# Optimization experiments

Measured on AMD Instinct MI355X. Metric: run time of the kernel, lower is better.

## Reference

```python
import jax, jax.numpy as jnp
import numpy as np

NUM_SUB = (128, 32)
NUM_NEI = (24, 24)
LN_EPS = 1e-5


def bilinear(fmap, pts):
    # fmap: [C,H,W]; pts: [P,2] as (y,x) normalized to [0,1]; align_corners=True
    C, H, W = fmap.shape
    gy = pts[:, 0] * (H - 1)
    gx = pts[:, 1] * (W - 1)
    y0 = jnp.floor(gy)
    x0 = jnp.floor(gx)
    wy = gy - y0
    wx = gx - x0
    y0i = jnp.clip(y0.astype(jnp.int32), 0, H - 1)
    y1i = jnp.clip(y0i + 1, 0, H - 1)
    x0i = jnp.clip(x0.astype(jnp.int32), 0, W - 1)
    x1i = jnp.clip(x0i + 1, 0, W - 1)
    v00 = fmap[:, y0i, x0i]
    v01 = fmap[:, y0i, x1i]
    v10 = fmap[:, y1i, x0i]
    v11 = fmap[:, y1i, x1i]
    out = (v00 * (1 - wy) * (1 - wx) + v01 * (1 - wy) * wx
           + v10 * wy * (1 - wx) + v11 * wy * wx)
    return out.T  # [P,C]


def fps(xyz, npoint):
    # farthest point sampling, deterministic start at index 0. xyz: [B,N,2]
    B, N, _ = xyz.shape
    bidx = jnp.arange(B)

    def step(carry, _):
        dist, far = carry
        c = xyz[bidx, far][:, None, :]            # [B,1,2]
        d = jnp.sum((xyz - c) ** 2, -1)           # [B,N]
        dist = jnp.minimum(dist, d)
        return (dist, jnp.argmax(dist, -1)), far

    init = (jnp.full((B, N), 1e10, xyz.dtype), jnp.zeros((B,), jnp.int32))
    _, idx = jax.lax.scan(step, init, None, length=npoint)
    return idx.T  # [B,npoint]


def sqdist(a, b):
    # a: [B,S,2], b: [B,N,2] -> [B,S,N]
    return (jnp.sum(a ** 2, -1)[..., None] + jnp.sum(b ** 2, -1)[:, None, :]
            - 2.0 * jnp.einsum('bsc,bnc->bsn', a, b))


def layernorm(x, g, b):
    m = jnp.mean(x, -1, keepdims=True)
    v = jnp.mean((x - m) ** 2, -1, keepdims=True)
    return (x - m) / jnp.sqrt(v + LN_EPS) * g + b


def setup_inputs() -> dict:
    key = jax.random.key(0)
    ks = jax.random.split(key, 8)
    B, N, C, H, W = 32, 512, 1024, 24, 24
    Dp = C + 2
    out_dim = 4096
    return {
        'feature_map': jax.random.normal(ks[0], (B, C, H, W), jnp.float32),
        'points': jax.random.uniform(ks[1], (B, N, 2), jnp.float32),
        'W_diff': jax.random.normal(ks[2], (2, Dp, Dp), jnp.float32) * 0.02,
        'b_diff': jnp.zeros((2, Dp), jnp.float32),
        'W_agg': jax.random.normal(ks[3], (2, C, 2 * Dp), jnp.float32) * 0.02,
        'b_agg': jnp.zeros((2, C), jnp.float32),
        'ln_g': jnp.ones((2, C), jnp.float32),
        'ln_b': jnp.zeros((2, C), jnp.float32),
        'W_flat': jax.random.normal(ks[4], (C, C * NUM_SUB[-1]), jnp.float32) * 0.02,
        'b_flat': jnp.zeros((C,), jnp.float32),
        'W_dim': jax.random.normal(ks[5], (out_dim, C), jnp.float32) * 0.02,
        'b_dim': jnp.zeros((out_dim,), jnp.float32),
    }


def reference(feature_map, points, W_diff, b_diff, W_agg, b_agg,
              ln_g, ln_b, W_flat, b_flat, W_dim, b_dim):
    B = points.shape[0]
    all_pts = points                              # [B,N,2]
    all_fea = jax.vmap(bilinear)(feature_map, points)  # [B,N,C]
    bidx = jnp.arange(B)[:, None, None]
    for i, (S, K) in enumerate(zip(NUM_SUB, NUM_NEI)):
        fi = fps(all_pts, S)                                   # [B,S]
        new_pts = jnp.take_along_axis(all_pts, fi[..., None], 1)   # [B,S,2]
        new_fea = jnp.take_along_axis(all_fea, fi[..., None], 1)   # [B,S,C]
        d2 = sqdist(new_pts, all_pts)                          # [B,S,N]
        _, idx = jax.lax.top_k(-d2, K)                         # [B,S,K]
        grp_pts = all_pts[bidx, idx]                           # [B,S,K,2]
        grp_fea = all_fea[bidx, idx]                           # [B,S,K,C]
        local = jnp.concatenate([grp_fea, grp_pts], -1)        # [B,S,K,C+2]
        anchor = jnp.concatenate([new_fea, new_pts], -1)[:, :, None, :]
        diff = jnp.einsum('bskd,od->bsko', local - anchor, W_diff[i]) + b_diff[i]
        gath = jnp.concatenate([diff, jnp.broadcast_to(anchor, diff.shape)], -1)
        # Conv1d(kernel=1) + ReLU + LayerNorm over channels
        h = jax.nn.relu(jnp.einsum('bskd,od->bsko', gath, W_agg[i]) + b_agg[i])
        h = layernorm(h, ln_g[i], ln_b[i])
        all_pts, all_fea = new_pts, jnp.mean(h, 2)             # mean pool over K
    x = all_fea.reshape(B, -1)
    x = x @ W_flat.T + b_flat
    return x @ W_dim.T + b_dim
```

## Files before the change

kernel.cpp:

```cpp
#include <hip/hip_runtime.h>


typedef float f32x4 __attribute__((ext_vector_type(4)));
typedef short bf16x8 __attribute__((ext_vector_type(8)));
typedef unsigned short u16;
typedef u16 u16x4 __attribute__((ext_vector_type(4)));
typedef unsigned int u32;
typedef u32 u32x4 __attribute__((ext_vector_type(4)));
typedef unsigned long long u64;

typedef const void __attribute__((address_space(1)))* gvp;
typedef void __attribute__((address_space(3)))* svp;

__device__ __forceinline__ u16 f2bf(float f) {
  union { float f; u32 u; } x; x.f = f;
  u32 r = x.u + 0x7fffu + ((x.u >> 16) & 1u);
  return (u16)(r >> 16);
}

#define KP 1056
#define NP0 1152

__device__ __forceinline__ float rl_f(float v, int lane) {
  return __int_as_float(__builtin_amdgcn_readlane(__float_as_int(v), lane));
}

template <int CTRL>
__device__ __forceinline__ float dpp_fmax(float v) {
  float o = __int_as_float(__builtin_amdgcn_update_dpp(
      (int)0xff800000 , __float_as_int(v), CTRL, 0xf, 0xf, false));
  return fmaxf(v, o);
}

template <int CTRL>
__device__ __forceinline__ float dpp_fmin(float v) {
  float o = __int_as_float(__builtin_amdgcn_update_dpp(
      0x7f800000 , __float_as_int(v), CTRL, 0xf, 0xf, false));
  return fminf(v, o);
}

template <int CTRL>
__device__ __forceinline__ float dpp_add(float v) {
  float o = __int_as_float(__builtin_amdgcn_update_dpp(
      0, __float_as_int(v), CTRL, 0xf, 0xf, false));
  return v + o;
}

__device__ __forceinline__ float wave_fmax63(float v) {
  v = dpp_fmax<0x111>(v);
  v = dpp_fmax<0x112>(v);
  v = dpp_fmax<0x114>(v);
  v = dpp_fmax<0x118>(v);
  v = dpp_fmax<0x142>(v);
  v = dpp_fmax<0x143>(v);
  return rl_f(v, 63);
}

__device__ __forceinline__ float wave_fmin63(float v) {
  v = dpp_fmin<0x111>(v);
  v = dpp_fmin<0x112>(v);
  v = dpp_fmin<0x114>(v);
  v = dpp_fmin<0x118>(v);
  v = dpp_fmin<0x142>(v);
  v = dpp_fmin<0x143>(v);
  return rl_f(v, 63);
}

__device__ __forceinline__ float wave_sum63(float v) {
  v = dpp_add<0x111>(v);
  v = dpp_add<0x112>(v);
  v = dpp_add<0x114>(v);
  v = dpp_add<0x118>(v);
  v = dpp_add<0x142>(v);
  v = dpp_add<0x143>(v);
  return v;
}

template <int PPL, int HS>
__device__ void fps_core(const float* __restrict__ pts, int* __restrict__ fi,
                         int Np, int S, int b, int lane, int s0, int s1,
                         float* __restrict__ dsave, int* __restrict__ fsave) {
  #pragma clang fp contract(off)
  float px[PPL], py[PPL], dist[PPL];
  #pragma unroll
  for (int j = 0; j < PPL; ++j) {
    int n = j * 64 + lane;
    px[j] = pts[((size_t)b * Np + n) * 2];
    py[j] = pts[((size_t)b * Np + n) * 2 + 1];
  }
  int far; float cx, cy;
  if (s0 == 0) {
    #pragma unroll
    for (int j = 0; j < PPL; ++j) dist[j] = 1e10f;
    far = 0;
    cx = rl_f(px[0], 0);
    cy = rl_f(py[0], 0);
  } else {
    #pragma unroll
    for (int j = 0; j < PPL; ++j) dist[j] = dsave[(size_t)b * Np + j * 64 + lane];
    far = fsave[b];
    cx = pts[((size_t)b * Np + far) * 2];
    cy = pts[((size_t)b * Np + far) * 2 + 1];
  }
  int hist[HS];
  #pragma unroll
  for (int h = 0; h < HS; ++h) hist[h] = 0;
  for (int s = s0; s < s1; ++s) {
    #pragma unroll
    for (int h = 0; h < HS; ++h)
      if ((s >> 6) == h && (s & 63) == lane) hist[h] = far;
    float tv[PPL]; int ti[PPL]; float tx[PPL], ty[PPL];
    #pragma unroll
    for (int j = 0; j < PPL; ++j) {
      float dx = px[j] - cx, dy = py[j] - cy;
      float d = dx * dx + dy * dy;
      float nd = fminf(dist[j], d);
      dist[j] = nd;
      tv[j] = nd; ti[j] = j * 64 + lane; tx[j] = px[j]; ty[j] = py[j];
    }
    #pragma unroll
    for (int w = PPL; w > 1; w >>= 1)
      #pragma unroll
      for (int j = 0; j < (w >> 1); ++j)
        if (tv[j + (w >> 1)] > tv[j]) {
          tv[j] = tv[j + (w >> 1)]; ti[j] = ti[j + (w >> 1)];
          tx[j] = tx[j + (w >> 1)]; ty[j] = ty[j + (w >> 1)];
        }
    float smax = wave_fmax63(tv[0]);
    u64 mask = __ballot(tv[0] == smax);
    int L = __builtin_ctzll(mask);
    int fidx = __builtin_amdgcn_readlane(ti[0], L);
    float fx = rl_f(tx[0], L), fy = rl_f(ty[0], L);
    u64 rest = mask & (mask - 1);
    if (__builtin_expect(rest != 0, 0)) {
      while (rest) {
        int L2 = __builtin_ctzll(rest);
        int c = __builtin_amdgcn_readlane(ti[0], L2);
        if (c < fidx) {
          fidx = c; fx = rl_f(tx[0], L2); fy = rl_f(ty[0], L2);
        }
        rest &= rest - 1;
      }
    }
    far = fidx; cx = fx; cy = fy;
  }
  if (s1 < S) {
    #pragma unroll
    for (int j = 0; j < PPL; ++j) dsave[(size_t)b * Np + j * 64 + lane] = dist[j];
    if (lane == 0) fsave[b] = far;
  }
  #pragma unroll
  for (int h = 0; h < HS; ++h) {
    int s = h * 64 + lane;
    if (s >= s0 && s < s1) fi[b * S + s] = hist[h];
  }
}

template <int PPL>
__device__ void knn_core(const float* __restrict__ qpts,
                         const float* __restrict__ rpts,
                         int* __restrict__ idxK, int Np, int S, int q, int lane) {
  #pragma clang fp contract(off)
  int b = q / S;
  float ax = qpts[(size_t)q * 2], ay = qpts[(size_t)q * 2 + 1];
  float a2 = ax * ax + ay * ay;
  float d2[PPL];
  #pragma unroll
  for (int j = 0; j < PPL; ++j) {
    int n = j * 64 + lane;
    float bx = rpts[((size_t)b * Np + n) * 2];
    float by = rpts[((size_t)b * Np + n) * 2 + 1];
    float b2 = bx * bx + by * by;
    float dot = ax * bx + ay * by;
    float t = a2 + b2;
    float m2 = 2.f * dot;
    d2[j] = t - m2;
  }
  int kreg = 0;
  for (int k = 0; k < 24; ++k) {
    float tv[PPL]; int ti[PPL];
    #pragma unroll
    for (int j = 0; j < PPL; ++j) { tv[j] = d2[j]; ti[j] = j * 64 + lane; }
    #pragma unroll
    for (int w = PPL; w > 1; w >>= 1)
      #pragma unroll
      for (int j = 0; j < (w >> 1); ++j)
        if (tv[j + (w >> 1)] < tv[j]) {
          tv[j] = tv[j + (w >> 1)]; ti[j] = ti[j + (w >> 1)];
        }
    float smin = wave_fmin63(tv[0]);
    u64 mask = __ballot(tv[0] == smin);
    int L = __builtin_ctzll(mask);
    int bs = __builtin_amdgcn_readlane(ti[0], L);
    u64 rest = mask & (mask - 1);
    if (__builtin_expect(rest != 0, 0)) {
      while (rest) {
        int L2 = __builtin_ctzll(rest);
        int c = __builtin_amdgcn_readlane(ti[0], L2);
        if (c < bs) bs = c;
        rest &= rest - 1;
      }
    }
    if (lane == k) kreg = bs;
    #pragma unroll
    for (int j = 0; j < PPL; ++j)
      if (j * 64 + lane == bs) d2[j] = 3.4e38f;
  }
  if (lane < 24) idxK[(size_t)q * 24 + lane] = kreg;
}

__global__ __launch_bounds__(256, 2) void bilinear_fused_kernel(const float* __restrict__ fmap,
                                                                const float* __restrict__ pts,
                                                                u16* __restrict__ X,
                                                                int* __restrict__ fi0,
                                                                float* __restrict__ fdist,
                                                                int* __restrict__ ffar) {
  if (blockIdx.y == 0) {
    if (blockIdx.x < 8)
      fps_core<8, 2>(pts, fi0, 512, 128, blockIdx.x * 4 + (threadIdx.x >> 6),
                     threadIdx.x & 63, 0, 48, fdist, ffar);
    return;
  }
  __shared__ float fmS[32][580];
  const int ct = blockIdx.x, b = blockIdx.y - 1;
  const int t = threadIdx.x;
  const float* src = fmap + ((size_t)b * 1024 + ct * 32) * 576;
  const int tr = t >> 3, ti = t & 7;
  #pragma unroll
  for (int j = 0; j < 18; ++j) {
    int c4 = j * 8 + ti;
    *(f32x4*)&fmS[tr][c4 * 4] = *(const f32x4*)(src + (size_t)tr * 576 + c4 * 4);
  }
  __syncthreads();
  #pragma unroll
  for (int pass = 0; pass < 2; ++pass) {
    const int n = pass * 256 + t;
    const int pidx = b * 512 + n;
    float p0 = pts[(size_t)pidx * 2], p1 = pts[(size_t)pidx * 2 + 1];
    float gy = p0 * 23.f, gx = p1 * 23.f;
    float y0f = floorf(gy), x0f = floorf(gx);
    float wy = gy - y0f, wx = gx - x0f;
    int y0 = (int)y0f; y0 = y0 < 0 ? 0 : (y0 > 23 ? 23 : y0);
    int x0 = (int)x0f; x0 = x0 < 0 ? 0 : (x0 > 23 ? 23 : x0);
    int y1 = y0 + 1 > 23 ? 23 : y0 + 1;
    int x1 = x0 + 1 > 23 ? 23 : x0 + 1;
    float w00 = (1.f - wy) * (1.f - wx), w01 = (1.f - wy) * wx;
    float w10 = wy * (1.f - wx), w11 = wy * wx;
    const int i00 = y0 * 24 + x0, i01 = y0 * 24 + x1;
    const int i10 = y1 * 24 + x0, i11 = y1 * 24 + x1;
    size_t ro = (size_t)pidx * KP + ct * 32;
    #pragma unroll
    for (int cq = 0; cq < 8; ++cq) {
      u16x4 o4;
      #pragma unroll
      for (int cc = 0; cc < 4; ++cc) {
        int c = cq * 4 + cc;
        float v = w00 * fmS[c][i00] + w01 * fmS[c][i01] +
                  w10 * fmS[c][i10] + w11 * fmS[c][i11];
        o4[cc] = f2bf(v);
      }
      *(u16x4*)(X + ro + cq * 4) = o4;
    }
    if (ct == 31) {
      size_t rb = (size_t)pidx * KP;
      X[rb + 1024] = f2bf(p0);
      X[rb + 1025] = f2bf(p1);
      #pragma unroll
      for (int z = 0; z < 15; ++z) ((u32*)(X + rb + 1026))[z] = 0;
    }
  }
}

__global__ __launch_bounds__(128) void gather_fi_kernel(const u16* __restrict__ Xsrc,
                                                        const float* __restrict__ pts,
                                                        const int* __restrict__ fi,
                                                        u16* __restrict__ Xg,
                                                        float* __restrict__ npts,
                                                        int Np, int S) {
  int q = blockIdx.x;
  int b = q / S;
  int t = threadIdx.x;
  int r = fi[q];
  const u32x4* src = (const u32x4*)(Xsrc + ((size_t)b * Np + r) * KP);
  u32x4* dst = (u32x4*)(Xg + (size_t)q * KP);
  dst[t] = src[t];
  int t2 = t + 128;
  if (t2 < 132) dst[t2] = src[t2];
  if (t == 0) {
    npts[(size_t)q * 2] = pts[((size_t)b * Np + r) * 2];
    npts[(size_t)q * 2 + 1] = pts[((size_t)b * Np + r) * 2 + 1];
  }
}

__global__ __launch_bounds__(256) void wd_transpose_kernel(const float* __restrict__ Wd,
                                                           u16* __restrict__ WdT) {
  __shared__ float tbuf[32][33];
  int tx = threadIdx.x & 31, ty = threadIdx.x >> 5;
  int ot = blockIdx.x * 32, dt = blockIdx.y * 32;
  #pragma unroll
  for (int j = 0; j < 4; ++j) {
    int o = ot + ty + 8 * j, d = dt + tx;
    tbuf[ty + 8 * j][tx] = (o < 1026 && d < 1026) ? Wd[(size_t)o * 1026 + d] : 0.f;
  }
  __syncthreads();
  #pragma unroll
  for (int j = 0; j < 4; ++j) {
    int d = dt + ty + 8 * j, o = ot + tx;
    if (o < KP) WdT[(size_t)d * KP + o] = f2bf(tbuf[tx][ty + 8 * j]);
  }
}

__global__ __launch_bounds__(256) void wagg_convert_kernel(const float* __restrict__ Wagg,
                                                           u16* __restrict__ Wa1,
                                                           u16* __restrict__ Wa2) {
  int c = blockIdx.x, t = threadIdx.x;
  const float* row = Wagg + (size_t)c * 2052;
  for (int d = t; d < KP; d += 256) {
    Wa1[(size_t)c * KP + d] = (d < 1026) ? f2bf(row[d]) : (u16)0;
    Wa2[(size_t)c * KP + d] = (d < 1026) ? f2bf(row[1026 + d]) : (u16)0;
  }
}

__global__ __launch_bounds__(256) void czero_kernel(const float* __restrict__ bdiff,
                                                    const float* __restrict__ Wagg,
                                                    const float* __restrict__ bagg,
                                                    float* __restrict__ czero) {
  int lane = threadIdx.x & 63, wv = threadIdx.x >> 6;
  int c = blockIdx.x * 4 + wv;
  float acc = 0.f;
  for (int o = lane; o < 1026; o += 64) acc += bdiff[o] * Wagg[(size_t)c * 2052 + o];
  #pragma unroll
  for (int off = 32; off; off >>= 1) acc += __shfl_xor(acc, off);
  if (lane == 0) czero[c] = acc + bagg[c];
}

template <int BF16OUT, int FPS_PPL, int FPS_HS, int SWZ, int KNN_PPL>
__global__ __launch_bounds__(256) void gemm_bt_kernel(const u16* __restrict__ A,
                                                      const u16* __restrict__ Bt,
                                                      void* __restrict__ Cout,
                                                      int M, int N, int K, int ldc, int nvalid,
                                                      const float* __restrict__ fpts,
                                                      int* __restrict__ ffi,
                                                      int fNp, int fS, int fs0, int fs1,
                                                      float* __restrict__ fdist,
                                                      int* __restrict__ ffar,
                                                      const float* __restrict__ kq,
                                                      const float* __restrict__ kr,
                                                      int* __restrict__ kidx,
                                                      int kNp, int kS, int kYoff) {
  const int tid = threadIdx.x;
  const int lane = tid & 63;
  const int wv = tid >> 6;
  const int FR = (FPS_PPL > 0) ? 1 : 0;
  if (FPS_PPL > 0 && blockIdx.y == 0) {
    if (blockIdx.x < 8)
      fps_core<FPS_PPL ? FPS_PPL : 1, FPS_HS>(fpts, ffi, fNp, fS,
                                              blockIdx.x * 4 + wv, lane, fs0, fs1,
                                              fdist, ffar);
    return;
  }
  if (KNN_PPL > 0 && (int)blockIdx.y >= kYoff) {
    int kb = ((int)blockIdx.y - kYoff) * gridDim.x + blockIdx.x;
    knn_core<KNN_PPL ? KNN_PPL : 1>(kq, kr, kidx, kNp, kS, kb * 4 + wv, lane);
    return;
  }
  __shared__ __align__(16) u16 As[128 * 32];
  __shared__ __align__(16) u16 Bs[128 * 32];
  int mt, nt;
  if (SWZ) {
    const int g = ((int)blockIdx.y - FR) * gridDim.x + blockIdx.x;
    const int MT = (KNN_PPL > 0 ? kYoff : (int)gridDim.y) - FR;
    const int cpx = MT >> 3;
    const int xcd = g & 7;
    const int r = g >> 3;
    mt = xcd * cpx + (r >> 3);
    nt = r & 7;
  } else {
    mt = (int)blockIdx.y - FR;
    nt = blockIdx.x;
  }
  const int m0 = mt * 128;
  const int n0 = nt * 128;
  const int wm = (wv >> 1) * 64;
  const int wn = (wv & 1) * 64;

  f32x4 acc[4][4];
  #pragma unroll
  for (int i = 0; i < 4; ++i)
    #pragma unroll
    for (int j = 0; j < 4; ++j)
      #pragma unroll
      for (int c = 0; c < 4; ++c) acc[i][j][c] = 0.f;

  const int ch0 = wv * 2;
  const int rin = lane >> 2;
  const int slot = lane & 3;
  const int cin = (slot ^ (rin & 3) ^ ((rin >> 2) & 3)) * 8;

  for (int k0 = 0; k0 < K; k0 += 32) {
    #pragma unroll
    for (int i = 0; i < 2; ++i) {
      const int ch = ch0 + i;
      const int row = ch * 16 + rin;
      const u16* ga = A + (size_t)(m0 + row) * K + (k0 + cin);
      const u16* gb = Bt + (size_t)(n0 + row) * K + (k0 + cin);
      __builtin_amdgcn_global_load_lds((gvp)ga, (svp)(As + ch * 512), 16, 0, 0);
      __builtin_amdgcn_global_load_lds((gvp)gb, (svp)(Bs + ch * 512), 16, 0, 0);
    }
    __syncthreads();
    const int rf = lane & 15;
    const int quad = lane >> 4;
    const int qs = (quad ^ (rf & 3) ^ ((rf >> 2) & 3)) * 8;
    bf16x8 af[4], bfv[4];
    #pragma unroll
    for (int mi = 0; mi < 4; ++mi)
      af[mi] = *(const bf16x8*)(As + (wm + mi * 16 + rf) * 32 + qs);
    #pragma unroll
    for (int ni = 0; ni < 4; ++ni)
      bfv[ni] = *(const bf16x8*)(Bs + (wn + ni * 16 + rf) * 32 + qs);
    #pragma unroll
    for (int mi = 0; mi < 4; ++mi)
      #pragma unroll
      for (int ni = 0; ni < 4; ++ni)
        acc[mi][ni] = __builtin_amdgcn_mfma_f32_16x16x32_bf16(af[mi], bfv[ni], acc[mi][ni], 0, 0, 0);
    __syncthreads();
  }

  const int rq = (lane >> 4) * 4;
  const int cf = lane & 15;
  #pragma unroll
  for (int mi = 0; mi < 4; ++mi) {
    #pragma unroll
    for (int ni = 0; ni < 4; ++ni) {
      const int col = n0 + wn + ni * 16 + cf;
      #pragma unroll
      for (int r = 0; r < 4; ++r) {
        const int row = m0 + wm + mi * 16 + rq + r;
        const float v = acc[mi][ni][r];
        if (BF16OUT) {
          if (col < nvalid) ((u16*)Cout)[(size_t)row * ldc + col] = f2bf(v);
        } else {
          ((float*)Cout)[(size_t)row * ldc + col] = v;
        }
      }
    }
  }
}

template <int MODE, int FPS_PPL, int FPS_HS>
__global__ __launch_bounds__(256) void h_epilogue_kernel(const float* __restrict__ Z1,
                                                         const float* __restrict__ Z2g,
                                                         const float* __restrict__ czero,
                                                         const int* __restrict__ idxK,
                                                         const int* __restrict__ fi,
                                                         const float* __restrict__ g,
                                                         const float* __restrict__ bb,
                                                         const float* __restrict__ npts,
                                                         void* __restrict__ outp,
                                                         int Np, int S, int cpx,
                                                         const float* __restrict__ fpts,
                                                         int* __restrict__ ffi,
                                                         int fNp, int fS) {
  const int t = threadIdx.x;
  const int lane = t & 63, wv = t >> 6;
  if (FPS_PPL > 0 && blockIdx.x < 8) {
    fps_core<FPS_PPL ? FPS_PPL : 1, FPS_HS>(fpts, ffi, fNp, fS,
                                            blockIdx.x * 4 + wv, lane, 0, fS,
                                            nullptr, nullptr);
    return;
  }
  const int bid = blockIdx.x - (FPS_PPL > 0 ? 8 : 0);
  const int sw = (bid & 7) * cpx + (bid >> 3);
  const int q = sw * 4 + wv;
  const int b = q / S;
  const int fiv = fi[q];
  const float* z2 = Z2g + (size_t)q * 1024;
  const float* zf = Z1 + ((size_t)b * Np + fiv) * 1024;
  const int ch = lane * 4;

  f32x4 base[4], gv[4], bv[4], acc[4];
  #pragma unroll
  for (int j = 0; j < 4; ++j) {
    f32x4 a = *(const f32x4*)(z2 + j * 256 + ch);
    f32x4 c = *(const f32x4*)(czero + j * 256 + ch);
    f32x4 f = *(const f32x4*)(zf + j * 256 + ch);
    #pragma unroll
    for (int c2 = 0; c2 < 4; ++c2) base[j][c2] = a[c2] + c[c2] - f[c2];
    gv[j] = *(const f32x4*)(g + j * 256 + ch);
    bv[j] = *(const f32x4*)(bb + j * 256 + ch);
    #pragma unroll
    for (int c2 = 0; c2 < 4; ++c2) acc[j][c2] = 0.f;
  }
  int nk = 0;
  if (lane < 24) nk = idxK[(size_t)q * 24 + lane];

  for (int k = 0; k < 24; ++k) {
    const int n = __builtin_amdgcn_readlane(nk, k);
    const float* zr = Z1 + ((size_t)b * Np + n) * 1024;
    f32x4 v[4];
    float s1 = 0.f, s2 = 0.f;
    #pragma unroll
    for (int j = 0; j < 4; ++j) {
      f32x4 r = *(const f32x4*)(zr + j * 256 + ch);
      #pragma unroll
      for (int c2 = 0; c2 < 4; ++c2) {
        float x = fmaxf(r[c2] + base[j][c2], 0.f);
        v[j][c2] = x;
        s1 += x;
        s2 += x * x;
      }
    }
    s1 = wave_sum63(s1);
    s2 = wave_sum63(s2);
    const float S1 = rl_f(s1, 63);
    const float S2 = rl_f(s2, 63);
    const float m = S1 * (1.f / 1024.f);
    const float var = S2 * (1.f / 1024.f) - m * m;
    const float rs = rsqrtf(var + 1e-5f);
    #pragma unroll
    for (int j = 0; j < 4; ++j)
      #pragma unroll
      for (int c2 = 0; c2 < 4; ++c2)
        acc[j][c2] += (v[j][c2] - m) * rs * gv[j][c2] + bv[j][c2];
  }

  u16x4 o4[4];
  #pragma unroll
  for (int j = 0; j < 4; ++j)
    #pragma unroll
    for (int c2 = 0; c2 < 4; ++c2) o4[j][c2] = f2bf(acc[j][c2] * (1.f / 24.f));

  if (MODE == 0) {
    u16* X = (u16*)outp;
    size_t ro = (size_t)q * KP;
    #pragma unroll
    for (int j = 0; j < 4; ++j) *(u16x4*)(X + ro + j * 256 + ch) = o4[j];
    if (lane == 0) {
      X[ro + 1024] = f2bf(npts[(size_t)q * 2]);
      X[ro + 1025] = f2bf(npts[(size_t)q * 2 + 1]);
    }
    if (lane < 15) ((u32*)(X + ro + 1026))[lane] = 0;
  } else {
    u16* X = (u16*)outp + (size_t)q * 1024;
    #pragma unroll
    for (int j = 0; j < 4; ++j) *(u16x4*)(X + j * 256 + ch) = o4[j];
  }
}

template <int KSBITS, int NST>
__global__ __launch_bounds__(256, 4) void mlp_mfma_kernel(const float* __restrict__ W,
                                                          const u16* __restrict__ Fb,
                                                          float* __restrict__ P, int K) {
  __shared__ __align__(16) float Asf[128 * 32];
  __shared__ __align__(16) u16 Fsb[32 * 40];
  const int tid = threadIdx.x, lane = tid & 63, wv = tid >> 6;
  const int ot = blockIdx.x >> KSBITS;
  const int ks = blockIdx.x & ((1 << KSBITS) - 1);
  const int m0 = ot * 128;
  const int k0b = ks * (NST * 32);
  const int arow = lane >> 3;
  const int agrp = lane & 7;
  const int rf = lane & 15, quad = lane >> 4;

  f32x4 acc[2][2];
  #pragma unroll
  for (int i = 0; i < 2; ++i)
    #pragma unroll
    for (int j = 0; j < 2; ++j)
      #pragma unroll
      for (int c = 0; c < 4; ++c) acc[i][j][c] = 0.f;

  for (int st = 0; st < NST; ++st) {
    const int k0 = k0b + st * 32;
    #pragma unroll
    for (int i = 0; i < 4; ++i) {
      const int row = wv * 32 + i * 8 + arow;
      const int g = agrp ^ (row & 7);
      const float* ga = W + (size_t)(m0 + row) * K + k0 + g * 4;
      __builtin_amdgcn_global_load_lds((gvp)ga, (svp)(Asf + (wv * 32 + i * 8) * 32), 16, 0, 0);
    }
    if (tid < 128) {
      const int fr = tid >> 2, fc = (tid & 3) * 8;
      u32x4 tmp = *(const u32x4*)(Fb + (size_t)fr * K + k0 + fc);
      *(u32x4*)(Fsb + fr * 40 + fc) = tmp;
    }
    __syncthreads();
    bf16x8 bfr[2];
    #pragma unroll
    for (int ni = 0; ni < 2; ++ni)
      bfr[ni] = *(const bf16x8*)(Fsb + (ni * 16 + rf) * 40 + quad * 8);
    #pragma unroll
    for (int mi = 0; mi < 2; ++mi) {
      const float* ap = Asf + (size_t)(wv * 32 + mi * 16 + rf) * 32;
      f32x4 a0 = *(const f32x4*)(ap + (((quad * 2) ^ (rf & 7)) * 4));
      f32x4 a1 = *(const f32x4*)(ap + (((quad * 2 + 1) ^ (rf & 7)) * 4));
      union { bf16x8 v; u16 h[8]; } af;
      #pragma unroll
      for (int c = 0; c < 4; ++c) { af.h[c] = f2bf(a0[c]); af.h[4 + c] = f2bf(a1[c]); }
      #pragma unroll
      for (int ni = 0; ni < 2; ++ni)
        acc[mi][ni] = __builtin_amdgcn_mfma_f32_16x16x32_bf16(af.v, bfr[ni], acc[mi][ni], 0, 0, 0);
    }
    __syncthreads();
  }

  float* Pb = P + (size_t)blockIdx.x * 4096;
  const int rq = (lane >> 4) * 4, cf = lane & 15;
  #pragma unroll
  for (int mi = 0; mi < 2; ++mi)
    #pragma unroll
    for (int ni = 0; ni < 2; ++ni)
      #pragma unroll
      for (int r = 0; r < 4; ++r)
        Pb[(wv * 32 + mi * 16 + rq + r) * 32 + ni * 16 + cf] = acc[mi][ni][r];
}

__global__ __launch_bounds__(256) void reduce_flat_kernel(const float* __restrict__ P,
                                                          const float* __restrict__ bias,
                                                          u16* __restrict__ x1bf) {
  int idx = blockIdx.x * 256 + threadIdx.x;
  int o = idx >> 5, b = idx & 31;
  float s = bias[o];
  const float* p = P + ((size_t)(o >> 7) * 64) * 4096 + (o & 127) * 32 + b;
  #pragma unroll 8
  for (int ks = 0; ks < 64; ++ks) s += p[(size_t)ks * 4096];
  x1bf[(size_t)b * 1024 + o] = f2bf(s);
}

__global__ __launch_bounds__(256) void reduce_dim_kernel(const float* __restrict__ P,
                                                         const float* __restrict__ bias,
                                                         float* __restrict__ out) {
  int idx = blockIdx.x * 256 + threadIdx.x;
  int o = idx >> 5, b = idx & 31;
  float s = bias[o];
  const float* p = P + ((size_t)(o >> 7) * 8) * 4096 + (o & 127) * 32 + b;
  #pragma unroll
  for (int ks = 0; ks < 8; ++ks) s += p[(size_t)ks * 4096];
  out[(size_t)b * 4096 + o] = s;
}

extern "C" void kernel_launch(void* const* d_in, const int* in_sizes, int n_in,
                              void* d_out, int out_size, void* d_ws, size_t ws_size,
                              hipStream_t stream) {
  const float* fmap  = (const float*)d_in[0];
  const float* pts   = (const float*)d_in[1];
  const float* Wdiff = (const float*)d_in[2];
  const float* bdiff = (const float*)d_in[3];
  const float* Wagg  = (const float*)d_in[4];
  const float* bagg  = (const float*)d_in[5];
  const float* lng   = (const float*)d_in[6];
  const float* lnb   = (const float*)d_in[7];
  const float* Wflat = (const float*)d_in[8];
  const float* bflat = (const float*)d_in[9];
  const float* Wdim  = (const float*)d_in[10];
  const float* bdim  = (const float*)d_in[11];
  float* out = (float*)d_out;

  char* w = (char*)d_ws;
  size_t off = 0;
  auto alloc = [&](size_t n) { char* p = w + off; off += (n + 255) & ~(size_t)255; return p; };

  float* Z1    = (float*)alloc(16384ull * 1024 * 4);
  float* Z2g   = (float*)alloc(4096ull * 1024 * 4);
  u16* Xbf0  = (u16*)alloc(16384ull * KP * 2);
  u16* X1bf  = (u16*)alloc(4096ull * KP * 2);
  u16* Xg    = (u16*)alloc(4096ull * KP * 2);
  u16* WdT   = (u16*)alloc((size_t)NP0 * KP * 2);
  u16* Wa1   = (u16*)alloc(1024ull * KP * 2);
  u16* Wa2   = (u16*)alloc(1024ull * KP * 2);
  u16* Wcomb = (u16*)alloc(1024ull * KP * 2);
  float* czero = (float*)alloc(1024 * 4);
  int* fi0   = (int*)alloc(32 * 128 * 4);
  int* fi1   = (int*)alloc(32 * 32 * 4);
  int* idx0  = (int*)alloc(32 * 128 * 24 * 4);
  int* idx1  = (int*)alloc(32 * 32 * 24 * 4);
  float* npts0 = (float*)alloc(32 * 128 * 2 * 4);
  float* npts1 = (float*)alloc(32 * 32 * 2 * 4);
  u16* fea2bf = (u16*)alloc(32ull * 32768 * 2);
  u16* x1bf   = (u16*)alloc(32ull * 1024 * 2);
  float* Pf   = (float*)alloc(512ull * 4096 * 4);
  float* Pd   = (float*)alloc(256ull * 4096 * 4);
  float* fdist = (float*)alloc(32ull * 512 * 4);
  int* ffar    = (int*)alloc(32 * 4);

  bilinear_fused_kernel<<<dim3(32, 33), 256, 0, stream>>>(fmap, pts, Xbf0, fi0, fdist, ffar);

  wd_transpose_kernel<<<dim3(33, 36), 256, 0, stream>>>(Wdiff, WdT);
  wagg_convert_kernel<<<1024, 256, 0, stream>>>(Wagg, Wa1, Wa2);
  czero_kernel<<<256, 256, 0, stream>>>(bdiff, Wagg, bagg, czero);
  gemm_bt_kernel<1, 0, 1, 0, 0><<<dim3(9, 8), 256, 0, stream>>>(
      Wa1, WdT, Wcomb, 1024, NP0, KP, KP, KP,
      nullptr, nullptr, 0, 0, 0, 0, nullptr, nullptr,
      nullptr, nullptr, nullptr, 0, 0, 0);
  gemm_bt_kernel<0, 8, 2, 1, 0><<<dim3(8, 129), 256, 0, stream>>>(
      Xbf0, Wcomb, Z1, 16384, 1024, KP, 1024, 1024,
      pts, fi0, 512, 128, 48, 128, fdist, ffar,
      nullptr, nullptr, nullptr, 0, 0, 0);
  gather_fi_kernel<<<4096, 128, 0, stream>>>(Xbf0, pts, fi0, Xg, npts0, 512, 128);
  gemm_bt_kernel<0, 0, 1, 1, 8><<<dim3(8, 160), 256, 0, stream>>>(
      Xg, Wa2, Z2g, 4096, 1024, KP, 1024, 1024,
      nullptr, nullptr, 0, 0, 0, 0, nullptr, nullptr,
      npts0, pts, idx0, 512, 128, 32);
  h_epilogue_kernel<0, 2, 1><<<1032, 256, 0, stream>>>(
      Z1, Z2g, czero, idx0, fi0, lng, lnb, npts0, X1bf, 512, 128, 128,
      npts0, fi1, 128, 32);

  wd_transpose_kernel<<<dim3(33, 36), 256, 0, stream>>>(Wdiff + 1026 * 1026, WdT);
  wagg_convert_kernel<<<1024, 256, 0, stream>>>(Wagg + 1024 * 2052, Wa1, Wa2);
  czero_kernel<<<256, 256, 0, stream>>>(bdiff + 1026, Wagg + 1024 * 2052, bagg + 1024, czero);
  gemm_bt_kernel<1, 0, 1, 0, 0><<<dim3(9, 8), 256, 0, stream>>>(
      Wa1, WdT, Wcomb, 1024, NP0, KP, KP, KP,
      nullptr, nullptr, 0, 0, 0, 0, nullptr, nullptr,
      nullptr, nullptr, nullptr, 0, 0, 0);
  gemm_bt_kernel<0, 0, 1, 1, 0><<<dim3(8, 32), 256, 0, stream>>>(
      X1bf, Wcomb, Z1, 4096, 1024, KP, 1024, 1024,
      nullptr, nullptr, 0, 0, 0, 0, nullptr, nullptr,
      nullptr, nullptr, nullptr, 0, 0, 0);
  gather_fi_kernel<<<1024, 128, 0, stream>>>(X1bf, npts0, fi1, Xg, npts1, 128, 32);
  gemm_bt_kernel<0, 0, 1, 1, 2><<<dim3(8, 40), 256, 0, stream>>>(
      Xg, Wa2, Z2g, 1024, 1024, KP, 1024, 1024,
      nullptr, nullptr, 0, 0, 0, 0, nullptr, nullptr,
      npts1, npts0, idx1, 128, 32, 8);
  h_epilogue_kernel<1, 0, 1><<<256, 256, 0, stream>>>(
      Z1, Z2g, czero, idx1, fi1, lng + 1024, lnb + 1024, npts1, fea2bf, 128, 32, 32,
      nullptr, nullptr, 0, 0);

  mlp_mfma_kernel<6, 16><<<512, 256, 0, stream>>>(Wflat, fea2bf, Pf, 32768);
  reduce_flat_kernel<<<128, 256, 0, stream>>>(Pf, bflat, x1bf);
  mlp_mfma_kernel<3, 4><<<256, 256, 0, stream>>>(Wdim, x1bf, Pd, 1024);
  reduce_dim_kernel<<<512, 256, 0, stream>>>(Pd, bdim, out);
}
```

Baseline: 623.9 us.

## Batch both stages' weight prep, fold row gather into GEMM, split FPS across kernels

Weight preprocessing for both stages (transpose, bf16 conversion, czero bias fold, Wcomb GEMM) is now done in fewer, batched launches. Stage-two weight prep no longer sits on the critical path between the stages. The separate gather_fi kernels are removed: the gather GEMMs index rows of the source activations through the FPS indices, and FPS writes the sampled point coordinates directly. The first-stage FPS is split into three segments (0-32, 32-56, 56-128) hidden behind the bilinear, Wcomb and first GEMM kernels. This trades fewer launches and less copy traffic for more scattered A-row loads and a larger weight workspace.

After: 551.4 us. 1.13x faster.

```diff
diff --git a/kernel.cpp b/kernel.cpp
--- a/kernel.cpp
+++ b/kernel.cpp
@@ -78,6 +78,7 @@
 
 template <int PPL, int HS>
 __device__ void fps_core(const float* __restrict__ pts, int* __restrict__ fi,
+                         float* __restrict__ npts,
                          int Np, int S, int b, int lane, int s0, int s1,
                          float* __restrict__ dsave, int* __restrict__ fsave) {
   #pragma clang fp contract(off)
@@ -152,7 +153,12 @@
   #pragma unroll
   for (int h = 0; h < HS; ++h) {
     int s = h * 64 + lane;
-    if (s >= s0 && s < s1) fi[b * S + s] = hist[h];
+    if (s >= s0 && s < s1) {
+      int hv = hist[h];
+      fi[b * S + s] = hv;
+      npts[(size_t)(b * S + s) * 2]     = pts[((size_t)b * Np + hv) * 2];
+      npts[(size_t)(b * S + s) * 2 + 1] = pts[((size_t)b * Np + hv) * 2 + 1];
+    }
   }
 }
 
@@ -209,16 +215,108 @@
   if (lane < 24) idxK[(size_t)q * 24 + lane] = kreg;
 }
 
+template <int BF16OUT, int IND>
+__device__ __forceinline__ void gemm_tile_body(const u16* __restrict__ A,
+                                               const u16* __restrict__ Bt,
+                                               void* __restrict__ Cout,
+                                               int K, int ldc, int nvalid,
+                                               int m0, int n0,
+                                               const int* __restrict__ find,
+                                               int iNp, int iS,
+                                               u16* __restrict__ As,
+                                               u16* __restrict__ Bs) {
+  const int tid = threadIdx.x;
+  const int lane = tid & 63;
+  const int wv = tid >> 6;
+  const int wm = (wv >> 1) * 64;
+  const int wn = (wv & 1) * 64;
+
+  f32x4 acc[4][4];
+  #pragma unroll
+  for (int i = 0; i < 4; ++i)
+    #pragma unroll
+    for (int j = 0; j < 4; ++j)
+      #pragma unroll
+      for (int c = 0; c < 4; ++c) acc[i][j][c] = 0.f;
+
+  const int ch0 = wv * 2;
+  const int rin = lane >> 2;
+  const int slot = lane & 3;
+  const int cin = (slot ^ (rin & 3) ^ ((rin >> 2) & 3)) * 8;
+
+  size_t aro[2];
+  #pragma unroll
+  for (int i = 0; i < 2; ++i) {
+    const int row = (ch0 + i) * 16 + rin;
+    if (IND) {
+      const int q = m0 + row;
+      aro[i] = (size_t)(q / iS) * iNp + find[q];
+    } else {
+      aro[i] = (size_t)(m0 + row);
+    }
+  }
+
+  for (int k0 = 0; k0 < K; k0 += 32) {
+    #pragma unroll
+    for (int i = 0; i < 2; ++i) {
+      const int ch = ch0 + i;
+      const int row = ch * 16 + rin;
+      const u16* ga = A + aro[i] * K + (k0 + cin);
+      const u16* gb = Bt + (size_t)(n0 + row) * K + (k0 + cin);
+      __builtin_amdgcn_global_load_lds((gvp)ga, (svp)(As + ch * 512), 16, 0, 0);
+      __builtin_amdgcn_global_load_lds((gvp)gb, (svp)(Bs + ch * 512), 16, 0, 0);
+    }
+    __syncthreads();
+    const int rf = lane & 15;
+    const int quad = lane >> 4;
+    const int qs = (quad ^ (rf & 3) ^ ((rf >> 2) & 3)) * 8;
+    bf16x8 af[4], bfv[4];
+    #pragma unroll
+    for (int mi = 0; mi < 4; ++mi)
+      af[mi] = *(const bf16x8*)(As + (wm + mi * 16 + rf) * 32 + qs);
+    #pragma unroll
+    for (int ni = 0; ni < 4; ++ni)
+      bfv[ni] = *(const bf16x8*)(Bs + (wn + ni * 16 + rf) * 32 + qs);
+    #pragma unroll
+    for (int mi = 0; mi < 4; ++mi)
+      #pragma unroll
+      for (int ni = 0; ni < 4; ++ni)
+        acc[mi][ni] = __builtin_amdgcn_mfma_f32_16x16x32_bf16(af[mi], bfv[ni], acc[mi][ni], 0, 0, 0);
+    __syncthreads();
+  }
+
+  const int rq = (lane >> 4) * 4;
+  const int cf = lane & 15;
+  #pragma unroll
+  for (int mi = 0; mi < 4; ++mi) {
+    #pragma unroll
+    for (int ni = 0; ni < 4; ++ni) {
+      const int col = n0 + wn + ni * 16 + cf;
+      #pragma unroll
+      for (int r = 0; r < 4; ++r) {
+        const int row = m0 + wm + mi * 16 + rq + r;
+        const float v = acc[mi][ni][r];
+        if (BF16OUT) {
+          if (col < nvalid) ((u16*)Cout)[(size_t)row * ldc + col] = f2bf(v);
+        } else {
+          ((float*)Cout)[(size_t)row * ldc + col] = v;
+        }
+      }
+    }
+  }
+}
+
 __global__ __launch_bounds__(256, 2) void bilinear_fused_kernel(const float* __restrict__ fmap,
                                                                 const float* __restrict__ pts,
                                                                 u16* __restrict__ X,
                                                                 int* __restrict__ fi0,
+                                                                float* __restrict__ npts0,
                                                                 float* __restrict__ fdist,
                                                                 int* __restrict__ ffar) {
   if (blockIdx.y == 0) {
     if (blockIdx.x < 8)
-      fps_core<8, 2>(pts, fi0, 512, 128, blockIdx.x * 4 + (threadIdx.x >> 6),
-                     threadIdx.x & 63, 0, 48, fdist, ffar);
+      fps_core<8, 2>(pts, fi0, npts0, 512, 128, blockIdx.x * 4 + (threadIdx.x >> 6),
+                     threadIdx.x & 63, 0, 32, fdist, ffar);
     return;
   }
   __shared__ float fmS[32][580];
@@ -271,76 +369,98 @@
   }
 }
 
-__global__ __launch_bounds__(128) void gather_fi_kernel(const u16* __restrict__ Xsrc,
-                                                        const float* __restrict__ pts,
-                                                        const int* __restrict__ fi,
-                                                        u16* __restrict__ Xg,
-                                                        float* __restrict__ npts,
-                                                        int Np, int S) {
-  int q = blockIdx.x;
-  int b = q / S;
-  int t = threadIdx.x;
-  int r = fi[q];
-  const u32x4* src = (const u32x4*)(Xsrc + ((size_t)b * Np + r) * KP);
-  u32x4* dst = (u32x4*)(Xg + (size_t)q * KP);
-  dst[t] = src[t];
-  int t2 = t + 128;
-  if (t2 < 132) dst[t2] = src[t2];
-  if (t == 0) {
-    npts[(size_t)q * 2] = pts[((size_t)b * Np + r) * 2];
-    npts[(size_t)q * 2 + 1] = pts[((size_t)b * Np + r) * 2 + 1];
-  }
-}
-
 __global__ __launch_bounds__(256) void wd_transpose_kernel(const float* __restrict__ Wd,
                                                            u16* __restrict__ WdT) {
   __shared__ float tbuf[32][33];
+  const float* Wds = Wd + (size_t)blockIdx.z * 1026 * 1026;
+  u16* WdTs = WdT + (size_t)blockIdx.z * NP0 * KP;
   int tx = threadIdx.x & 31, ty = threadIdx.x >> 5;
   int ot = blockIdx.x * 32, dt = blockIdx.y * 32;
   #pragma unroll
   for (int j = 0; j < 4; ++j) {
     int o = ot + ty + 8 * j, d = dt + tx;
-    tbuf[ty + 8 * j][tx] = (o < 1026 && d < 1026) ? Wd[(size_t)o * 1026 + d] : 0.f;
+    tbuf[ty + 8 * j][tx] = (o < 1026 && d < 1026) ? Wds[(size_t)o * 1026 + d] : 0.f;
   }
   __syncthreads();
   #pragma unroll
   for (int j = 0; j < 4; ++j) {
     int d = dt + ty + 8 * j, o = ot + tx;
-    if (o < KP) WdT[(size_t)d * KP + o] = f2bf(tbuf[tx][ty + 8 * j]);
-  }
-}
-
-__global__ __launch_bounds__(256) void wagg_convert_kernel(const float* __restrict__ Wagg,
-                                                           u16* __restrict__ Wa1,
-                                                           u16* __restrict__ Wa2) {
-  int c = blockIdx.x, t = threadIdx.x;
-  const float* row = Wagg + (size_t)c * 2052;
+    if (o < KP) WdTs[(size_t)d * KP + o] = f2bf(tbuf[tx][ty + 8 * j]);
+  }
+}
+
+__global__ __launch_bounds__(256) void waggcz_kernel(const float* __restrict__ Wagg,
+                                                     const float* __restrict__ bdiff,
+                                                     const float* __restrict__ bagg,
+                                                     u16* __restrict__ Wa1,
+                                                     u16* __restrict__ Wa2,
+                                                     float* __restrict__ czero) {
+  __shared__ float red[4];
+  const int bid = blockIdx.x;
+  const int stage = bid >> 10, c = bid & 1023;
+  const float* row = Wagg + (size_t)stage * 1024 * 2052 + (size_t)c * 2052;
+  const float* bd = bdiff + stage * 1026;
+  u16* wa1 = Wa1 + (size_t)stage * 1024 * KP + (size_t)c * KP;
+  u16* wa2 = Wa2 + (size_t)stage * 1024 * KP + (size_t)c * KP;
+  const int t = threadIdx.x;
+  float acc = 0.f;
   for (int d = t; d < KP; d += 256) {
-    Wa1[(size_t)c * KP + d] = (d < 1026) ? f2bf(row[d]) : (u16)0;
-    Wa2[(size_t)c * KP + d] = (d < 1026) ? f2bf(row[1026 + d]) : (u16)0;
-  }
-}
-
-__global__ __launch_bounds__(256) void czero_kernel(const float* __restrict__ bdiff,
-                                                    const float* __restrict__ Wagg,
-                                                    const float* __restrict__ bagg,
-                                                    float* __restrict__ czero) {
-  int lane = threadIdx.x & 63, wv = threadIdx.x >> 6;
-  int c = blockIdx.x * 4 + wv;
-  float acc = 0.f;
-  for (int o = lane; o < 1026; o += 64) acc += bdiff[o] * Wagg[(size_t)c * 2052 + o];
-  #pragma unroll
-  for (int off = 32; off; off >>= 1) acc += __shfl_xor(acc, off);
-  if (lane == 0) czero[c] = acc + bagg[c];
-}
-
-template <int BF16OUT, int FPS_PPL, int FPS_HS, int SWZ, int KNN_PPL>
+    if (d < 1026) {
+      float v1 = row[d];
+      float v2 = row[1026 + d];
+      wa1[d] = f2bf(v1);
+      wa2[d] = f2bf(v2);
+      acc += bd[d] * v1;
+    } else {
+      wa1[d] = 0;
+      wa2[d] = 0;
+    }
+  }
+  float s = wave_sum63(acc);
+  const int lane = t & 63, wv = t >> 6;
+  if (lane == 63) red[wv] = s;
+  __syncthreads();
+  if (t == 0)
+    czero[(size_t)stage * 1024 + c] = red[0] + red[1] + red[2] + red[3] + bagg[stage * 1024 + c];
+}
+
+__global__ __launch_bounds__(256) void wcomb_dual_kernel(const u16* __restrict__ Wa1,
+                                                         const u16* __restrict__ WdT,
+                                                         u16* __restrict__ Wcomb,
+                                                         const float* __restrict__ fpts,
+                                                         int* __restrict__ ffi,
+                                                         float* __restrict__ fnpts,
+                                                         float* __restrict__ fdist,
+                                                         int* __restrict__ ffar) {
+  __shared__ __align__(16) u16 As[128 * 32];
+  __shared__ __align__(16) u16 Bs[128 * 32];
+  const int wv = threadIdx.x >> 6, lane = threadIdx.x & 63;
+  if (blockIdx.y == 0) {
+    if (blockIdx.x < 8)
+      fps_core<8, 2>(fpts, ffi, fnpts, 512, 128, blockIdx.x * 4 + wv, lane, 32, 56,
+                     fdist, ffar);
+    return;
+  }
+  const int y = blockIdx.y - 1;
+  const int stage = y >> 3;
+  const int mt = y & 7;
+  const u16* A = Wa1 + (size_t)stage * 1024 * KP;
+  const u16* B = WdT + (size_t)stage * NP0 * KP;
+  u16* C = Wcomb + (size_t)stage * 1024 * KP;
+  gemm_tile_body<1, 0>(A, B, C, KP, KP, KP, mt * 128, blockIdx.x * 128,
+                       nullptr, 0, 0, As, Bs);
+}
+
+template <int BF16OUT, int FPS_PPL, int FPS_HS, int SWZ, int KNN_PPL, int IND>
 __global__ __launch_bounds__(256) void gemm_bt_kernel(const u16* __restrict__ A,
                                                       const u16* __restrict__ Bt,
                                                       void* __restrict__ Cout,
-                                                      int M, int N, int K, int ldc, int nvalid,
+                                                      int K, int ldc, int nvalid,
+                                                      const int* __restrict__ find,
+                                                      int iNp, int iS,
                                                       const float* __restrict__ fpts,
                                                       int* __restrict__ ffi,
+                                                      float* __restrict__ fnpts,
                                                       int fNp, int fS, int fs0, int fs1,
                                                       float* __restrict__ fdist,
                                                       int* __restrict__ ffar,
@@ -354,7 +474,7 @@
   const int FR = (FPS_PPL > 0) ? 1 : 0;
   if (FPS_PPL > 0 && blockIdx.y == 0) {
     if (blockIdx.x < 8)
-      fps_core<FPS_PPL ? FPS_PPL : 1, FPS_HS>(fpts, ffi, fNp, fS,
+      fps_core<FPS_PPL ? FPS_PPL : 1, FPS_HS>(fpts, ffi, fnpts, fNp, fS,
                                               blockIdx.x * 4 + wv, lane, fs0, fs1,
                                               fdist, ffar);
     return;
@@ -379,72 +499,8 @@
     mt = (int)blockIdx.y - FR;
     nt = blockIdx.x;
   }
-  const int m0 = mt * 128;
-  const int n0 = nt * 128;
-  const int wm = (wv >> 1) * 64;
-  const int wn = (wv & 1) * 64;
-
-  f32x4 acc[4][4];
-  #pragma unroll
-  for (int i = 0; i < 4; ++i)
-    #pragma unroll
-    for (int j = 0; j < 4; ++j)
-      #pragma unroll
-      for (int c = 0; c < 4; ++c) acc[i][j][c] = 0.f;
-
-  const int ch0 = wv * 2;
-  const int rin = lane >> 2;
-  const int slot = lane & 3;
-  const int cin = (slot ^ (rin & 3) ^ ((rin >> 2) & 3)) * 8;
-
-  for (int k0 = 0; k0 < K; k0 += 32) {
-    #pragma unroll
-    for (int i = 0; i < 2; ++i) {
-      const int ch = ch0 + i;
-      const int row = ch * 16 + rin;
-      const u16* ga = A + (size_t)(m0 + row) * K + (k0 + cin);
-      const u16* gb = Bt + (size_t)(n0 + row) * K + (k0 + cin);
-      __builtin_amdgcn_global_load_lds((gvp)ga, (svp)(As + ch * 512), 16, 0, 0);
-      __builtin_amdgcn_global_load_lds((gvp)gb, (svp)(Bs + ch * 512), 16, 0, 0);
-    }
-    __syncthreads();
-    const int rf = lane & 15;
-    const int quad = lane >> 4;
-    const int qs = (quad ^ (rf & 3) ^ ((rf >> 2) & 3)) * 8;
-    bf16x8 af[4], bfv[4];
-    #pragma unroll
-    for (int mi = 0; mi < 4; ++mi)
-      af[mi] = *(const bf16x8*)(As + (wm + mi * 16 + rf) * 32 + qs);
-    #pragma unroll
-    for (int ni = 0; ni < 4; ++ni)
-      bfv[ni] = *(const bf16x8*)(Bs + (wn + ni * 16 + rf) * 32 + qs);
-    #pragma unroll
-    for (int mi = 0; mi < 4; ++mi)
-      #pragma unroll
-      for (int ni = 0; ni < 4; ++ni)
-        acc[mi][ni] = __builtin_amdgcn_mfma_f32_16x16x32_bf16(af[mi], bfv[ni], acc[mi][ni], 0, 0, 0);
-    __syncthreads();
-  }
-
-  const int rq = (lane >> 4) * 4;
-  const int cf = lane & 15;
-  #pragma unroll
-  for (int mi = 0; mi < 4; ++mi) {
-    #pragma unroll
-    for (int ni = 0; ni < 4; ++ni) {
-      const int col = n0 + wn + ni * 16 + cf;
-      #pragma unroll
-      for (int r = 0; r < 4; ++r) {
-        const int row = m0 + wm + mi * 16 + rq + r;
-        const float v = acc[mi][ni][r];
-        if (BF16OUT) {
-          if (col < nvalid) ((u16*)Cout)[(size_t)row * ldc + col] = f2bf(v);
-        } else {
-          ((float*)Cout)[(size_t)row * ldc + col] = v;
-        }
-      }
-    }
-  }
+  gemm_tile_body<BF16OUT, IND>(A, Bt, Cout, K, ldc, nvalid, mt * 128, nt * 128,
+                               find, iNp, iS, As, Bs);
 }
 
 template <int MODE, int FPS_PPL, int FPS_HS>
@@ -460,11 +516,12 @@
                                                          int Np, int S, int cpx,
                                                          const float* __restrict__ fpts,
                                                          int* __restrict__ ffi,
+                                                         float* __restrict__ fnpts,
                                                          int fNp, int fS) {
   const int t = threadIdx.x;
   const int lane = t & 63, wv = t >> 6;
   if (FPS_PPL > 0 && blockIdx.x < 8) {
-    fps_core<FPS_PPL ? FPS_PPL : 1, FPS_HS>(fpts, ffi, fNp, fS,
+    fps_core<FPS_PPL ? FPS_PPL : 1, FPS_HS>(fpts, ffi, fnpts, fNp, fS,
                                             blockIdx.x * 4 + wv, lane, 0, fS,
                                             nullptr, nullptr);
     return;
@@ -664,12 +721,11 @@
   float* Z2g   = (float*)alloc(4096ull * 1024 * 4);
   u16* Xbf0  = (u16*)alloc(16384ull * KP * 2);
   u16* X1bf  = (u16*)alloc(4096ull * KP * 2);
-  u16* Xg    = (u16*)alloc(4096ull * KP * 2);
-  u16* WdT   = (u16*)alloc((size_t)NP0 * KP * 2);
-  u16* Wa1   = (u16*)alloc(1024ull * KP * 2);
-  u16* Wa2   = (u16*)alloc(1024ull * KP * 2);
-  u16* Wcomb = (u16*)alloc(1024ull * KP * 2);
-  float* czero = (float*)alloc(1024 * 4);
+  u16* WdT   = (u16*)alloc(2ull * NP0 * KP * 2);
+  u16* Wa1   = (u16*)alloc(2ull * 1024 * KP * 2);
+  u16* Wa2   = (u16*)alloc(2ull * 1024 * KP * 2);
+  u16* Wcomb = (u16*)alloc(2ull * 1024 * KP * 2);
+  float* czero = (float*)alloc(2 * 1024 * 4);
   int* fi0   = (int*)alloc(32 * 128 * 4);
   int* fi1   = (int*)alloc(32 * 32 * 4);
   int* idx0  = (int*)alloc(32 * 128 * 24 * 4);
@@ -683,47 +739,38 @@
   float* fdist = (float*)alloc(32ull * 512 * 4);
   int* ffar    = (int*)alloc(32 * 4);
 
-  bilinear_fused_kernel<<<dim3(32, 33), 256, 0, stream>>>(fmap, pts, Xbf0, fi0, fdist, ffar);
-
-  wd_transpose_kernel<<<dim3(33, 36), 256, 0, stream>>>(Wdiff, WdT);
-  wagg_convert_kernel<<<1024, 256, 0, stream>>>(Wagg, Wa1, Wa2);
-  czero_kernel<<<256, 256, 0, stream>>>(bdiff, Wagg, bagg, czero);
-  gemm_bt_kernel<1, 0, 1, 0, 0><<<dim3(9, 8), 256, 0, stream>>>(
-      Wa1, WdT, Wcomb, 1024, NP0, KP, KP, KP,
-      nullptr, nullptr, 0, 0, 0, 0, nullptr, nullptr,
+  bilinear_fused_kernel<<<dim3(32, 33), 256, 0, stream>>>(fmap, pts, Xbf0, fi0, npts0,
+                                                          fdist, ffar);
+  wd_transpose_kernel<<<dim3(33, 36, 2), 256, 0, stream>>>(Wdiff, WdT);
+  waggcz_kernel<<<2048, 256, 0, stream>>>(Wagg, bdiff, bagg, Wa1, Wa2, czero);
+  wcomb_dual_kernel<<<dim3(9, 17), 256, 0, stream>>>(Wa1, WdT, Wcomb, pts, fi0, npts0,
+                                                     fdist, ffar);
+  gemm_bt_kernel<0, 8, 2, 1, 0, 0><<<dim3(8, 129), 256, 0, stream>>>(
+      Xbf0, Wcomb, Z1, KP, 1024, 1024,
+      nullptr, 0, 0,
+      pts, fi0, npts0, 512, 128, 56, 128, fdist, ffar,
       nullptr, nullptr, nullptr, 0, 0, 0);
-  gemm_bt_kernel<0, 8, 2, 1, 0><<<dim3(8, 129), 256, 0, stream>>>(
-      Xbf0, Wcomb, Z1, 16384, 1024, KP, 1024, 1024,
-      pts, fi0, 512, 128, 48, 128, fdist, ffar,
-      nullptr, nullptr, nullptr, 0, 0, 0);
-  gather_fi_kernel<<<4096, 128, 0, stream>>>(Xbf0, pts, fi0, Xg, npts0, 512, 128);
-  gemm_bt_kernel<0, 0, 1, 1, 8><<<dim3(8, 160), 256, 0, stream>>>(
-      Xg, Wa2, Z2g, 4096, 1024, KP, 1024, 1024,
-      nullptr, nullptr, 0, 0, 0, 0, nullptr, nullptr,
+  gemm_bt_kernel<0, 0, 1, 1, 8, 1><<<dim3(8, 160), 256, 0, stream>>>(
+      Xbf0, Wa2, Z2g, KP, 1024, 1024,
+      fi0, 512, 128,
+      nullptr, nullptr, nullptr, 0, 0, 0, 0, nullptr, nullptr,
       npts0, pts, idx0, 512, 128, 32);
   h_epilogue_kernel<0, 2, 1><<<1032, 256, 0, stream>>>(
       Z1, Z2g, czero, idx0, fi0, lng, lnb, npts0, X1bf, 512, 128, 128,
-      npts0, fi1, 128, 32);
-
-  wd_transpose_kernel<<<dim3(33, 36), 256, 0, stream>>>(Wdiff + 1026 * 1026, WdT);
-  wagg_convert_kernel<<<1024, 256, 0, stream>>>(Wagg + 1024 * 2052, Wa1, Wa2);
-  czero_kernel<<<256, 256, 0, stream>>>(bdiff + 1026, Wagg + 1024 * 2052, bagg + 1024, czero);
-  gemm_bt_kernel<1, 0, 1, 0, 0><<<dim3(9, 8), 256, 0, stream>>>(
-      Wa1, WdT, Wcomb, 1024, NP0, KP, KP, KP,
-      nullptr, nullptr, 0, 0, 0, 0, nullptr, nullptr,
+      npts0, fi1, npts1, 128, 32);
+  gemm_bt_kernel<0, 0, 1, 1, 0, 0><<<dim3(8, 32), 256, 0, stream>>>(
+      X1bf, Wcomb + 1024ull * KP, Z1, KP, 1024, 1024,
+      nullptr, 0, 0,
+      nullptr, nullptr, nullptr, 0, 0, 0, 0, nullptr, nullptr,
       nullptr, nullptr, nullptr, 0, 0, 0);
-  gemm_bt_kernel<0, 0, 1, 1, 0><<<dim3(8, 32), 256, 0, stream>>>(
-      X1bf, Wcomb, Z1, 4096, 1024, KP, 1024, 1024,
-      nullptr, nullptr, 0, 0, 0, 0, nullptr, nullptr,
-      nullptr, nullptr, nullptr, 0, 0, 0);
-  gather_fi_kernel<<<1024, 128, 0, stream>>>(X1bf, npts0, fi1, Xg, npts1, 128, 32);
-  gemm_bt_kernel<0, 0, 1, 1, 2><<<dim3(8, 40), 256, 0, stream>>>(
-      Xg, Wa2, Z2g, 1024, 1024, KP, 1024, 1024,
-      nullptr, nullptr, 0, 0, 0, 0, nullptr, nullptr,
+  gemm_bt_kernel<0, 0, 1, 1, 2, 1><<<dim3(8, 40), 256, 0, stream>>>(
+      X1bf, Wa2 + 1024ull * KP, Z2g, KP, 1024, 1024,
+      fi1, 128, 32,
+      nullptr, nullptr, nullptr, 0, 0, 0, 0, nullptr, nullptr,
       npts1, npts0, idx1, 128, 32, 8);
   h_epilogue_kernel<1, 0, 1><<<256, 256, 0, stream>>>(
-      Z1, Z2g, czero, idx1, fi1, lng + 1024, lnb + 1024, npts1, fea2bf, 128, 32, 32,
-      nullptr, nullptr, 0, 0);
+      Z1, Z2g, czero + 1024, idx1, fi1, lng + 1024, lnb + 1024, npts1, fea2bf,
+      128, 32, 32, nullptr, nullptr, nullptr, 0, 0);
 
   mlp_mfma_kernel<6, 16><<<512, 256, 0, stream>>>(Wflat, fea2bf, Pf, 32768);
   reduce_flat_kernel<<<128, 256, 0, stream>>>(Pf, bflat, x1bf);
```
